# Kernel tuning notes

Measured on AMD Instinct MI355X. Metric: run time of the kernel, lower is better.

## Reference

```python
import jax, jax.numpy as jnp
import numpy as np

B = 4096  # number of graphs (segments)
H = 256   # hidden_aff = hidden_comp = hidden_prot
NEG = -1e30

def leaky(x):
    return jax.nn.leaky_relu(x, 0.1)

def _lin(key, fin, fout):
    k1, k2 = jax.random.split(key)
    lim = 1.0 / np.sqrt(fin)
    W = jax.random.uniform(k1, (fin, fout), jnp.float32, -lim, lim)
    b = jax.random.uniform(k2, (fout,), jnp.float32, -lim, lim)
    return W, b

def setup_inputs() -> dict:
    key = jax.random.key(0)
    ks = jax.random.split(key, 16)
    N = 262144
    comp_feature = jax.random.normal(ks[0], (N, H), jnp.float32)
    prot_feature = jax.random.normal(ks[1], (N, H), jnp.float32)
    batch_comp = jnp.sort(jax.random.randint(ks[2], (N,), 0, B, jnp.int32))
    batch_prot = jnp.sort(jax.random.randint(ks[3], (N,), 0, B, jnp.int32))
    c_aff_W, c_aff_b = _lin(ks[4], H, H)
    c_sup_W, c_sup_b = _lin(ks[5], H, H)
    p_aff_W, p_aff_b = _lin(ks[6], H, H)
    raw_W1, raw_b1 = _lin(ks[7], 3 * H, H)
    raw_W2, raw_b2 = _lin(ks[8], H, H)
    alpha_W1, alpha_b1 = _lin(ks[9], 3 * H, H)
    alpha_W2, alpha_b2 = _lin(ks[10], H, 1)
    out_W1, out_b1 = _lin(ks[11], H, H)
    out_W2, out_b2 = _lin(ks[12], H, 1)
    return dict(comp_feature=comp_feature, prot_feature=prot_feature,
                batch_comp=batch_comp, batch_prot=batch_prot,
                c_aff_W=c_aff_W, c_aff_b=c_aff_b, c_sup_W=c_sup_W, c_sup_b=c_sup_b,
                p_aff_W=p_aff_W, p_aff_b=p_aff_b,
                raw_W1=raw_W1, raw_b1=raw_b1, raw_W2=raw_W2, raw_b2=raw_b2,
                alpha_W1=alpha_W1, alpha_b1=alpha_b1, alpha_W2=alpha_W2, alpha_b2=alpha_b2,
                out_W1=out_W1, out_b1=out_b1, out_W2=out_W2, out_b2=out_b2)

def reference(comp_feature, prot_feature, batch_comp, batch_prot,
              c_aff_W, c_aff_b, c_sup_W, c_sup_b, p_aff_W, p_aff_b,
              raw_W1, raw_b1, raw_W2, raw_b2,
              alpha_W1, alpha_b1, alpha_W2, alpha_b2,
              out_W1, out_b1, out_W2, out_b2):
    comp_emb = leaky(comp_feature @ c_aff_W + c_aff_b)           # [N, H]
    prot_emb = leaky(prot_feature @ p_aff_W + p_aff_b)           # [N, H]
    prot_pool = jax.ops.segment_max(prot_emb, batch_prot, num_segments=B)  # [B, H]
    supe = jax.ops.segment_sum(leaky(comp_feature @ c_sup_W + c_sup_b),
                               batch_comp, num_segments=B)       # [B, H]
    feat = jnp.concatenate([comp_emb, supe[batch_comp], prot_pool[batch_comp]], axis=1)  # [N, 3H]
    raw = leaky(feat @ raw_W1 + raw_b1) @ raw_W2 + raw_b2        # [N, H]
    prealpha = leaky(feat @ alpha_W1 + alpha_b1) @ alpha_W2 + alpha_b2  # [N, 1]
    # scatter softmax over graphs
    seg_max = jax.ops.segment_max(prealpha, batch_comp, num_segments=B)
    a_exp = jnp.exp(prealpha - seg_max[batch_comp])
    a_sum = jax.ops.segment_sum(a_exp, batch_comp, num_segments=B) + 1e-6
    alpha = a_exp / a_sum[batch_comp]                            # [N, 1]
    vector = jax.ops.segment_sum(raw * alpha, batch_comp, num_segments=B)  # [B, H]
    affinity_pred = leaky(vector @ out_W1 + out_b1) @ out_W2 + out_b2      # [B, 1]
    return vector, alpha, affinity_pred
```

## Files before the change

kernel.cpp:

```cpp
#include <hip/hip_runtime.h>
#include <cstddef>
#include <cstdint>

#define HDIM 256
#define BSEG 4096

typedef __bf16 bf16x8 __attribute__((ext_vector_type(8)));
typedef float f32x4 __attribute__((ext_vector_type(4)));

__device__ __forceinline__ float leaky(float x) { return x >= 0.f ? x : 0.1f * x; }
__device__ __forceinline__ float bf2f(ushort u) {
    return __builtin_bit_cast(float, (uint32_t)u << 16);
}
__device__ __forceinline__ ushort f2bf(float f) {
    uint32_t x = __builtin_bit_cast(uint32_t, f);
    return (ushort)((x + 0x7fffu + ((x >> 16) & 1u)) >> 16);
}
__device__ __forceinline__ bf16x8 pack8(float4 a, float4 b) {
    union { ushort s[8]; bf16x8 v; } u;
    u.s[0] = f2bf(a.x); u.s[1] = f2bf(a.y); u.s[2] = f2bf(a.z); u.s[3] = f2bf(a.w);
    u.s[4] = f2bf(b.x); u.s[5] = f2bf(b.y); u.s[6] = f2bf(b.z); u.s[7] = f2bf(b.w);
    return u.v;
}
__device__ __forceinline__ void store_bf4(ushort* p, float v0, float v1, float v2, float v3) {
    ushort4 o; o.x = f2bf(v0); o.y = f2bf(v1); o.z = f2bf(v2); o.w = f2bf(v3);
    *(ushort4*)p = o;
}

__device__ __forceinline__ void gld16(const ushort* g, ushort* lds) {
    __builtin_amdgcn_global_load_lds(
        (const __attribute__((address_space(1))) uint32_t*)g,
        (__attribute__((address_space(3))) uint32_t*)lds, 16, 0, 0);
}
__device__ __forceinline__ void gld16f(const float* g, float* lds) {
    __builtin_amdgcn_global_load_lds(
        (const __attribute__((address_space(1))) uint32_t*)g,
        (__attribute__((address_space(3))) uint32_t*)lds, 16, 0, 0);
}

__global__ void seg_bounds_k(const int* __restrict__ bc, const int* __restrict__ bp,
                             int* __restrict__ sc, int* __restrict__ sp, int n, int nb)
{
    int t = blockIdx.x * blockDim.x + threadIdx.x;
    if (t >= 2 * (nb + 1)) return;
    bool isc = (t <= nb);
    const int* a = isc ? bc : bp;
    int v = isc ? t : t - (nb + 1);
    int lo = 0, hi = n;
    while (lo < hi) { int mid = (lo + hi) >> 1; if (a[mid] < v) lo = mid + 1; else hi = mid; }
    if (isc) sc[t] = lo; else sp[t - (nb + 1)] = lo;
}

__global__ __launch_bounds__(256) void wt_cast_all(
    const float* __restrict__ s0, const float* __restrict__ s1,
    const float* __restrict__ s2, const float* __restrict__ s3,
    const float* __restrict__ s4, const float* __restrict__ s5,
    ushort* __restrict__ d0, ushort* __restrict__ d1, ushort* __restrict__ d2,
    ushort* __restrict__ d3, ushort* __restrict__ d4, ushort* __restrict__ d5)
{
    int m = blockIdx.x >> 4, tile = blockIdx.x & 15;
    const float* s = m == 0 ? s0 : m == 1 ? s1 : m == 2 ? s2 : m == 3 ? s3 : m == 4 ? s4 : s5;
    ushort*      d = m == 0 ? d0 : m == 1 ? d1 : m == 2 ? d2 : m == 3 ? d3 : m == 4 ? d4 : d5;
    int r0 = (tile >> 2) * 64, c0 = (tile & 3) * 64;
    __shared__ ushort t[64][72];
    int cc = threadIdx.x & 63, rr = threadIdx.x >> 6;
    for (int r = rr; r < 64; r += 4) t[cc][r] = f2bf(s[(size_t)(r0 + r) * 256 + c0 + cc]);
    __syncthreads();
    for (int r = rr; r < 64; r += 4) d[(size_t)(c0 + r) * 256 + r0 + cc] = t[r][cc];
}

template<bool LEAKYACT, bool ROWBIAS, bool AFP32, bool ALPHADOT, int YT>
__global__ __launch_bounds__(512) void mg2(
    const void* __restrict__ Av, const ushort* __restrict__ WT,
    const float* __restrict__ bias0, const float* __restrict__ bias1,
    const float* __restrict__ rt0, const float* __restrict__ rt1,
    const int* __restrict__ idx,
    ushort* __restrict__ out0, ushort* __restrict__ out1,
    const float* __restrict__ w2, float* __restrict__ pre)
{
    __shared__ __attribute__((aligned(16))) ushort Bs[2][256 * 32];
    __shared__ __attribute__((aligned(16))) char AsRaw[2][AFP32 ? 128 * 32 * 4 : 128 * 32 * 2];
    __shared__ float pb[128][4];

    const int tid = threadIdx.x;
    const int l = tid & 63, w = tid >> 6;

    const uint nwg = gridDim.x, orig = blockIdx.x;
    const uint swz = (orig & 7) * (nwg >> 3) + (orig >> 3);
    const int bx = (int)(swz / YT), cb = (int)(swz % YT);
    const int row0 = bx * 128, colb = cb * 256;

    const float*  Af = (const float*)Av;
    const ushort* Ah = (const ushort*)Av;

    const int sB0 = w * 128 + l;
    const int rB0 = sB0 >> 2,        rB1 = (sB0 + 64) >> 2;
    const int qB0 = (sB0 & 3) ^ ((rB0 >> 1) & 3), qB1 = ((sB0 + 64) & 3) ^ ((rB1 >> 1) & 3);
    const ushort* srcB0 = WT + (size_t)(colb + rB0) * HDIM + qB0 * 8;
    const ushort* srcB1 = WT + (size_t)(colb + rB1) * HDIM + qB1 * 8;
    const int sA0 = w * 128 + l;
    const int rA0 = sA0 >> 3,        rA1 = (sA0 + 64) >> 3;
    const int qA0 = (sA0 & 7) ^ (rA0 & 7), qA1 = ((sA0 + 64) & 7) ^ (rA1 & 7);
    const float* fsrc0 = Af + (size_t)(row0 + rA0) * HDIM + qA0 * 4;
    const float* fsrc1 = Af + (size_t)(row0 + rA1) * HDIM + qA1 * 4;
    const int rH = tid >> 2, qH = (tid & 3) ^ ((rH >> 1) & 3);
    const ushort* hsrc = Ah + (size_t)(row0 + rH) * HDIM + qH * 8;

    const int wr = (w >> 2) * 64, wc = (w & 3) * 64;
    const int lr = l & 15, lt = l >> 4;

    f32x4 acc[4][4] = {};

#define STAGE(buf, k0) do { \
        gld16(srcB0 + (k0), &Bs[buf][sB0 * 8]); \
        gld16(srcB1 + (k0), &Bs[buf][(sB0 + 64) * 8]); \
        if (AFP32) { \
            gld16f(fsrc0 + (k0), &((float*)AsRaw[buf])[sA0 * 4]); \
            gld16f(fsrc1 + (k0), &((float*)AsRaw[buf])[(sA0 + 64) * 4]); \
        } else { \
            gld16(hsrc + (k0), &((ushort*)AsRaw[buf])[tid * 8]); \
        } \
    } while (0)

#define COMPUTE(buf) do { \
        bf16x8 af[4], bv[4]; \
        _Pragma("unroll") \
        for (int m = 0; m < 4; ++m) { \
            const int row = wr + m * 16 + lr; \
            if (AFP32) { \
                const float* Ab = (const float*)AsRaw[buf]; \
                const int q0 = (2 * lt) ^ (row & 7), q1 = (2 * lt + 1) ^ (row & 7); \
                float4 x = *(const float4*)&Ab[row * 32 + q0 * 4]; \
                float4 y = *(const float4*)&Ab[row * 32 + q1 * 4]; \
                af[m] = pack8(x, y); \
            } else { \
                const ushort* Ab = (const ushort*)AsRaw[buf]; \
                const int q = lt ^ ((row >> 1) & 3); \
                af[m] = *(const bf16x8*)&Ab[row * 32 + q * 8]; \
            } \
        } \
        _Pragma("unroll") \
        for (int n = 0; n < 4; ++n) { \
            const int brow = wc + n * 16 + lr; \
            const int q = lt ^ ((brow >> 1) & 3); \
            bv[n] = *(const bf16x8*)&Bs[buf][brow * 32 + q * 8]; \
        } \
        _Pragma("unroll") \
        for (int m = 0; m < 4; ++m) \
            _Pragma("unroll") \
            for (int n = 0; n < 4; ++n) \
                acc[m][n] = __builtin_amdgcn_mfma_f32_16x16x32_bf16(bv[n], af[m], acc[m][n], 0, 0, 0); \
    } while (0)

    STAGE(0, 0);
    __syncthreads();
    int cur = 0;
    #pragma unroll
    for (int t = 1; t < 8; ++t) {
        STAGE(cur ^ 1, t * 32);
        COMPUTE(cur);
        __syncthreads();
        cur ^= 1;
    }
    COMPUTE(cur);

#undef STAGE
#undef COMPUTE

    if (ALPHADOT && cb == 1) {
        #pragma unroll
        for (int m = 0; m < 4; ++m) {
            const int row = row0 + wr + m * 16 + lr;
            const float* rrow = rt1 + (size_t)idx[row] * HDIM;
            float p = 0.f;
            #pragma unroll
            for (int n = 0; n < 4; ++n) {
                const int c = wc + n * 16 + (lt << 2);
                float4 r4 = *(const float4*)&rrow[c];
                float4 w4 = *(const float4*)&w2[c];
                float v0 = acc[m][n][0] + r4.x, v1 = acc[m][n][1] + r4.y;
                float v2 = acc[m][n][2] + r4.z, v3 = acc[m][n][3] + r4.w;
                if (LEAKYACT) { v0 = leaky(v0); v1 = leaky(v1); v2 = leaky(v2); v3 = leaky(v3); }
                p += v0 * w4.x + v1 * w4.y + v2 * w4.z + v3 * w4.w;
            }
            p += __shfl_xor(p, 16);
            p += __shfl_xor(p, 32);
            if (lt == 0) pb[wr + m * 16 + lr][w & 3] = p;
        }
        __syncthreads();
        if (tid < 128) pre[row0 + tid] = pb[tid][0] + pb[tid][1] + pb[tid][2] + pb[tid][3];
    } else {
        const float* bias = (YT == 2 && cb == 1) ? bias1 : bias0;
        const float* rtab = (YT == 2 && cb == 1) ? rt1 : rt0;
        ushort* outp = (YT == 2 && cb == 1) ? out1 : out0;
        #pragma unroll
        for (int m = 0; m < 4; ++m) {
            const int row = row0 + wr + m * 16 + lr;
            const float* rrow = nullptr;
            if (ROWBIAS) rrow = rtab + (size_t)idx[row] * HDIM;
            #pragma unroll
            for (int n = 0; n < 4; ++n) {
                const int c = wc + n * 16 + (lt << 2);
                float v0 = acc[m][n][0], v1 = acc[m][n][1], v2 = acc[m][n][2], v3 = acc[m][n][3];
                if (bias) {
                    float4 b4 = *(const float4*)&bias[c];
                    v0 += b4.x; v1 += b4.y; v2 += b4.z; v3 += b4.w;
                }
                if (ROWBIAS) {
                    float4 r4 = *(const float4*)&rrow[c];
                    v0 += r4.x; v1 += r4.y; v2 += r4.z; v3 += r4.w;
                }
                if (LEAKYACT) { v0 = leaky(v0); v1 = leaky(v1); v2 = leaky(v2); v3 = leaky(v3); }
                store_bf4(&outp[(size_t)row * HDIM + c], v0, v1, v2, v3);
            }
        }
    }
}

__global__ __launch_bounds__(256) void gemm64_2(
    const float* __restrict__ A, const float* __restrict__ A2,
    const float* __restrict__ Wb_r, const float* __restrict__ Wc_r, const float* __restrict__ bias_r,
    const float* __restrict__ Wb_a, const float* __restrict__ Wc_a, const float* __restrict__ bias_a,
    float* __restrict__ Cr, float* __restrict__ Ca)
{
    const int K = HDIM, NO = HDIM;
    const float* W  = blockIdx.z ? Wb_a : Wb_r;
    const float* W2 = blockIdx.z ? Wc_a : Wc_r;
    const float* bias = blockIdx.z ? bias_a : bias_r;
    float* C = blockIdx.z ? Ca : Cr;

    __shared__ float As [16][68];
    __shared__ float Bs [16][68];
    __shared__ float As2[16][68];
    __shared__ float Bs2[16][68];

    const int tid = threadIdx.x;
    const int tx = tid & 15, ty = tid >> 4;
    const int row0 = blockIdx.x * 64, col0 = blockIdx.y * 64;

    const int lr = tid >> 2;
    const int lk = (tid & 3) << 2;
    const int bk = tid >> 4;
    const int bj = (tid & 15) << 2;

    float acc[4][4] = {};

    for (int k0 = 0; k0 < K; k0 += 16) {
        float4 a4 = *(const float4*)&A[(size_t)(row0 + lr) * K + k0 + lk];
        As[lk + 0][lr] = a4.x; As[lk + 1][lr] = a4.y;
        As[lk + 2][lr] = a4.z; As[lk + 3][lr] = a4.w;
        *(float4*)&Bs[bk][bj] = *(const float4*)&W[(size_t)(k0 + bk) * NO + col0 + bj];
        float4 c4 = *(const float4*)&A2[(size_t)(row0 + lr) * K + k0 + lk];
        As2[lk + 0][lr] = c4.x; As2[lk + 1][lr] = c4.y;
        As2[lk + 2][lr] = c4.z; As2[lk + 3][lr] = c4.w;
        *(float4*)&Bs2[bk][bj] = *(const float4*)&W2[(size_t)(k0 + bk) * NO + col0 + bj];
        __syncthreads();
        #pragma unroll
        for (int kk = 0; kk < 16; ++kk) {
            float4 av = *(const float4*)&As[kk][ty << 2];
            float4 bv = *(const float4*)&Bs[kk][tx << 2];
            float a_[4] = {av.x, av.y, av.z, av.w};
            float b_[4] = {bv.x, bv.y, bv.z, bv.w};
            #pragma unroll
            for (int i = 0; i < 4; ++i)
                #pragma unroll
                for (int j = 0; j < 4; ++j)
                    acc[i][j] += a_[i] * b_[j];
            float4 av2 = *(const float4*)&As2[kk][ty << 2];
            float4 bv2 = *(const float4*)&Bs2[kk][tx << 2];
            float c_[4] = {av2.x, av2.y, av2.z, av2.w};
            float d_[4] = {bv2.x, bv2.y, bv2.z, bv2.w};
            #pragma unroll
            for (int i = 0; i < 4; ++i)
                #pragma unroll
                for (int j = 0; j < 4; ++j)
                    acc[i][j] += c_[i] * d_[j];
        }
        __syncthreads();
    }

    #pragma unroll
    for (int i = 0; i < 4; ++i) {
        int row = row0 + (ty << 2) + i;
        float vv[4];
        #pragma unroll
        for (int j = 0; j < 4; ++j) {
            int col = col0 + (tx << 2) + j;
            vv[j] = acc[i][j] + bias[col];
        }
        float4 o; o.x = vv[0]; o.y = vv[1]; o.z = vv[2]; o.w = vv[3];
        *(float4*)&C[(size_t)row * NO + col0 + (tx << 2)] = o;
    }
}

template<bool ISMAX>
__global__ __launch_bounds__(256) void seg_reduce8(const ushort* __restrict__ in,
        const int* __restrict__ starts, float* __restrict__ out)
{
    __shared__ float part[8][HDIM];
    const int b = blockIdx.x, tid = threadIdx.x;
    const int sub = tid & 31, r = tid >> 5;
    const int s = starts[b], e = starts[b + 1];
    float a[8];
    #pragma unroll
    for (int j = 0; j < 8; ++j) a[j] = ISMAX ? -INFINITY : 0.f;
    for (int i = s + r; i < e; i += 8) {
        uint4 v = *(const uint4*)&in[(size_t)i * HDIM + sub * 8];
        float f[8] = { bf2f((ushort)v.x), bf2f((ushort)(v.x >> 16)),
                       bf2f((ushort)v.y), bf2f((ushort)(v.y >> 16)),
                       bf2f((ushort)v.z), bf2f((ushort)(v.z >> 16)),
                       bf2f((ushort)v.w), bf2f((ushort)(v.w >> 16)) };
        #pragma unroll
        for (int j = 0; j < 8; ++j) a[j] = ISMAX ? fmaxf(a[j], f[j]) : (a[j] + f[j]);
    }
    #pragma unroll
    for (int j = 0; j < 8; ++j) part[r][sub * 8 + j] = a[j];
    __syncthreads();
    float res = part[0][tid];
    #pragma unroll
    for (int j = 1; j < 8; ++j) res = ISMAX ? fmaxf(res, part[j][tid]) : (res + part[j][tid]);
    out[(size_t)b * HDIM + tid] = res;
}

__global__ __launch_bounds__(64) void seg_softmax_k(const float* __restrict__ pre,
        const int* __restrict__ starts, float* __restrict__ alpha)
{
    int b = blockIdx.x, lane = threadIdx.x;
    int s = starts[b], e = starts[b + 1];
    float m = -INFINITY;
    for (int i = s + lane; i < e; i += 64) m = fmaxf(m, pre[i]);
    #pragma unroll
    for (int off = 32; off; off >>= 1) m = fmaxf(m, __shfl_xor(m, off));
    float sum = 0.f;
    for (int i = s + lane; i < e; i += 64) sum += expf(pre[i] - m);
    #pragma unroll
    for (int off = 32; off; off >>= 1) sum += __shfl_xor(sum, off);
    sum += 1e-6f;
    for (int i = s + lane; i < e; i += 64) alpha[i] = expf(pre[i] - m) / sum;
}

__global__ __launch_bounds__(256) void seg_wsum8(const ushort* __restrict__ raw,
        const float* __restrict__ alpha, const int* __restrict__ starts,
        float* __restrict__ vec)
{
    __shared__ float part[8][HDIM];
    const int b = blockIdx.x, tid = threadIdx.x;
    const int sub = tid & 31, r = tid >> 5;
    const int s = starts[b], e = starts[b + 1];
    float a[8] = {};
    for (int i = s + r; i < e; i += 8) {
        float al = alpha[i];
        uint4 v = *(const uint4*)&raw[(size_t)i * HDIM + sub * 8];
        a[0] += bf2f((ushort)v.x) * al;        a[1] += bf2f((ushort)(v.x >> 16)) * al;
        a[2] += bf2f((ushort)v.y) * al;        a[3] += bf2f((ushort)(v.y >> 16)) * al;
        a[4] += bf2f((ushort)v.z) * al;        a[5] += bf2f((ushort)(v.z >> 16)) * al;
        a[6] += bf2f((ushort)v.w) * al;        a[7] += bf2f((ushort)(v.w >> 16)) * al;
    }
    #pragma unroll
    for (int j = 0; j < 8; ++j) part[r][sub * 8 + j] = a[j];
    __syncthreads();
    float res = 0.f;
    #pragma unroll
    for (int j = 0; j < 8; ++j) res += part[j][tid];
    vec[(size_t)b * HDIM + tid] = res;
}

__global__ __launch_bounds__(256) void affinity_k(const float* __restrict__ vec,
        const float* __restrict__ W1, const float* __restrict__ b1,
        const float* __restrict__ W2, const float* __restrict__ b2,
        float* __restrict__ out)
{
    __shared__ float v[HDIM];
    __shared__ float red[4];
    int b = blockIdx.x, t = threadIdx.x;
    v[t] = vec[(size_t)b * HDIM + t];
    __syncthreads();
    float h = 0.f;
    #pragma unroll 8
    for (int k = 0; k < HDIM; ++k) h += v[k] * W1[(size_t)k * HDIM + t];
    h += b1[t];
    h = leaky(h);
    float p = h * W2[t];
    #pragma unroll
    for (int off = 32; off; off >>= 1) p += __shfl_down(p, off);
    int lane = t & 63, wid = t >> 6;
    if (lane == 0) red[wid] = p;
    __syncthreads();
    if (t == 0) out[b] = red[0] + red[1] + red[2] + red[3] + b2[0];
}

extern "C" void kernel_launch(void* const* d_in, const int* in_sizes, int n_in,
                              void* d_out, int out_size, void* d_ws, size_t ws_size,
                              hipStream_t stream)
{
    const int N = in_sizes[2];
    const int H = HDIM;
    const int B = BSEG;

    const float* comp   = (const float*)d_in[0];
    const float* prot   = (const float*)d_in[1];
    const int*   bc     = (const int*)d_in[2];
    const int*   bp     = (const int*)d_in[3];
    const float* c_aff_W = (const float*)d_in[4];
    const float* c_aff_b = (const float*)d_in[5];
    const float* c_sup_W = (const float*)d_in[6];
    const float* c_sup_b = (const float*)d_in[7];
    const float* p_aff_W = (const float*)d_in[8];
    const float* p_aff_b = (const float*)d_in[9];
    const float* raw_W1  = (const float*)d_in[10];
    const float* raw_b1  = (const float*)d_in[11];
    const float* raw_W2  = (const float*)d_in[12];
    const float* raw_b2  = (const float*)d_in[13];
    const float* alpha_W1 = (const float*)d_in[14];
    const float* alpha_b1 = (const float*)d_in[15];
    const float* alpha_W2 = (const float*)d_in[16];
    const float* out_W1  = (const float*)d_in[18];
    const float* out_b1  = (const float*)d_in[19];
    const float* out_W2  = (const float*)d_in[20];
    const float* out_b2  = (const float*)d_in[21];

    const size_t NBIG = (size_t)N * H;
    const size_t SSEG = (size_t)B * H;

    char* p = (char*)d_ws;
    ushort* e1 = (ushort*)p; p += NBIG * 2;
    ushort* e2 = (ushort*)p; p += NBIG * 2;
    ushort* e3 = (ushort*)p; p += NBIG * 2;
    float* supe = (float*)p;  p += SSEG * 4;
    float* pool = (float*)p;  p += SSEG * 4;
    float* gr   = (float*)p;  p += SSEG * 4;
    float* ga   = (float*)p;  p += SSEG * 4;
    float* pre  = (float*)p;  p += (size_t)N * 4;
    ushort* WT1 = (ushort*)p; p += (size_t)512 * 256 * 2;
    ushort* WTp = (ushort*)p; p += (size_t)256 * 256 * 2;
    ushort* WT2 = (ushort*)p; p += (size_t)512 * 256 * 2;
    ushort* WTr = (ushort*)p; p += (size_t)256 * 256 * 2;
    int* sc = (int*)p; p += (size_t)(B + 1) * 4;
    int* sp = (int*)p; p += (size_t)(B + 1) * 4;
    if ((size_t)(p - (char*)d_ws) > ws_size) return;

    ushort* h1   = e3;
    ushort* rawb = e2;

    float* out_vec   = (float*)d_out;
    float* out_alpha = out_vec + SSEG;
    float* out_aff   = out_alpha + N;

    dim3 blk(256), blk5(512);

    seg_bounds_k<<<(2 * (B + 1) + 255) / 256, blk, 0, stream>>>(bc, bp, sc, sp, N, B);
    wt_cast_all<<<6 * 16, blk, 0, stream>>>(
        c_aff_W, c_sup_W, p_aff_W, raw_W1, alpha_W1, raw_W2,
        WT1, WT1 + 65536, WTp, WT2, WT2 + 65536, WTr);

    mg2<true, false, true, false, 2><<<dim3(N / 128 * 2), blk5, 0, stream>>>(
        comp, WT1, c_aff_b, c_sup_b, nullptr, nullptr, nullptr, e1, e2, nullptr, nullptr);
    mg2<true, false, true, false, 1><<<dim3(N / 128), blk5, 0, stream>>>(
        prot, WTp, p_aff_b, nullptr, nullptr, nullptr, nullptr, e3, nullptr, nullptr, nullptr);
    seg_reduce8<false><<<B, blk, 0, stream>>>(e2, sc, supe);
    seg_reduce8<true ><<<B, blk, 0, stream>>>(e3, sp, pool);
    gemm64_2<<<dim3(B / 64, 4, 2), blk, 0, stream>>>(supe, pool,
        raw_W1 + H * H, raw_W1 + 2 * H * H, raw_b1,
        alpha_W1 + H * H, alpha_W1 + 2 * H * H, alpha_b1, gr, ga);
    mg2<true, true, false, true, 2><<<dim3(N / 128 * 2), blk5, 0, stream>>>(
        e1, WT2, nullptr, nullptr, gr, ga, bc, h1, nullptr, alpha_W2, pre);
    seg_softmax_k<<<B, dim3(64), 0, stream>>>(pre, sc, out_alpha);
    mg2<false, false, false, false, 1><<<dim3(N / 128), blk5, 0, stream>>>(
        h1, WTr, raw_b2, nullptr, nullptr, nullptr, nullptr, rawb, nullptr, nullptr, nullptr);
    seg_wsum8<<<B, blk, 0, stream>>>(rawb, out_alpha, sc, out_vec);
    affinity_k<<<B, blk, 0, stream>>>(out_vec, out_W1, out_b1, out_W2, out_b2, out_aff);
}
```

Baseline: 755.1 us.

## Reorder raw_W2 after segment weighted sum and convert fp32 A tiles to bf16

The raw_W2 projection is linear, so the alpha-weighted segment sum is now taken over the hidden activations h1 first. The W2 matmul then runs per graph on B rows instead of N rows, with raw_b2 scaled by the alpha mass per segment, which the softmax kernel now writes out. This removes one full N×256×256 GEMM and its intermediate buffer. Separately, fp32 A operands are now read into registers, converted to bf16 and written to LDS once per tile, halving LDS footprint and removing per-MFMA repacking, at the cost of losing async global-to-LDS loads for A.

```diff
diff --git a/kernel.cpp b/kernel.cpp
--- a/kernel.cpp
+++ b/kernel.cpp
@@ -28,11 +28,6 @@
 }
 
 __device__ __forceinline__ void gld16(const ushort* g, ushort* lds) {
-    __builtin_amdgcn_global_load_lds(
-        (const __attribute__((address_space(1))) uint32_t*)g,
-        (__attribute__((address_space(3))) uint32_t*)lds, 16, 0, 0);
-}
-__device__ __forceinline__ void gld16f(const float* g, float* lds) {
     __builtin_amdgcn_global_load_lds(
         (const __attribute__((address_space(1))) uint32_t*)g,
         (__attribute__((address_space(3))) uint32_t*)lds, 16, 0, 0);
@@ -54,13 +49,13 @@
 __global__ __launch_bounds__(256) void wt_cast_all(
     const float* __restrict__ s0, const float* __restrict__ s1,
     const float* __restrict__ s2, const float* __restrict__ s3,
-    const float* __restrict__ s4, const float* __restrict__ s5,
+    const float* __restrict__ s4,
     ushort* __restrict__ d0, ushort* __restrict__ d1, ushort* __restrict__ d2,
-    ushort* __restrict__ d3, ushort* __restrict__ d4, ushort* __restrict__ d5)
+    ushort* __restrict__ d3, ushort* __restrict__ d4)
 {
     int m = blockIdx.x >> 4, tile = blockIdx.x & 15;
-    const float* s = m == 0 ? s0 : m == 1 ? s1 : m == 2 ? s2 : m == 3 ? s3 : m == 4 ? s4 : s5;
-    ushort*      d = m == 0 ? d0 : m == 1 ? d1 : m == 2 ? d2 : m == 3 ? d3 : m == 4 ? d4 : d5;
+    const float* s = m == 0 ? s0 : m == 1 ? s1 : m == 2 ? s2 : m == 3 ? s3 : s4;
+    ushort*      d = m == 0 ? d0 : m == 1 ? d1 : m == 2 ? d2 : m == 3 ? d3 : d4;
     int r0 = (tile >> 2) * 64, c0 = (tile & 3) * 64;
     __shared__ ushort t[64][72];
     int cc = threadIdx.x & 63, rr = threadIdx.x >> 6;
@@ -70,7 +65,7 @@
 }
 
 template<bool LEAKYACT, bool ROWBIAS, bool AFP32, bool ALPHADOT, int YT>
-__global__ __launch_bounds__(512) void mg2(
+__global__ __launch_bounds__(512) void mg3(
     const void* __restrict__ Av, const ushort* __restrict__ WT,
     const float* __restrict__ bias0, const float* __restrict__ bias1,
     const float* __restrict__ rt0, const float* __restrict__ rt1,
@@ -79,7 +74,7 @@
     const float* __restrict__ w2, float* __restrict__ pre)
 {
     __shared__ __attribute__((aligned(16))) ushort Bs[2][256 * 32];
-    __shared__ __attribute__((aligned(16))) char AsRaw[2][AFP32 ? 128 * 32 * 4 : 128 * 32 * 2];
+    __shared__ __attribute__((aligned(16))) ushort As[2][128 * 32];
     __shared__ float pb[128][4];
 
     const int tid = threadIdx.x;
@@ -98,28 +93,19 @@
     const int qB0 = (sB0 & 3) ^ ((rB0 >> 1) & 3), qB1 = ((sB0 + 64) & 3) ^ ((rB1 >> 1) & 3);
     const ushort* srcB0 = WT + (size_t)(colb + rB0) * HDIM + qB0 * 8;
     const ushort* srcB1 = WT + (size_t)(colb + rB1) * HDIM + qB1 * 8;
-    const int sA0 = w * 128 + l;
-    const int rA0 = sA0 >> 3,        rA1 = (sA0 + 64) >> 3;
-    const int qA0 = (sA0 & 7) ^ (rA0 & 7), qA1 = ((sA0 + 64) & 7) ^ (rA1 & 7);
-    const float* fsrc0 = Af + (size_t)(row0 + rA0) * HDIM + qA0 * 4;
-    const float* fsrc1 = Af + (size_t)(row0 + rA1) * HDIM + qA1 * 4;
-    const int rH = tid >> 2, qH = (tid & 3) ^ ((rH >> 1) & 3);
-    const ushort* hsrc = Ah + (size_t)(row0 + rH) * HDIM + qH * 8;
+    const int srow = tid >> 2, sj = tid & 3;
+    const int lj = sj ^ ((srow >> 1) & 3);
+    const float*  fsrcA = Af + (size_t)(row0 + srow) * HDIM + lj * 8;
+    const ushort* hsrcA = Ah + (size_t)(row0 + srow) * HDIM + lj * 8;
 
     const int wr = (w >> 2) * 64, wc = (w & 3) * 64;
     const int lr = l & 15, lt = l >> 4;
 
     f32x4 acc[4][4] = {};
 
-#define STAGE(buf, k0) do { \
+#define STAGE_B(buf, k0) do { \
         gld16(srcB0 + (k0), &Bs[buf][sB0 * 8]); \
         gld16(srcB1 + (k0), &Bs[buf][(sB0 + 64) * 8]); \
-        if (AFP32) { \
-            gld16f(fsrc0 + (k0), &((float*)AsRaw[buf])[sA0 * 4]); \
-            gld16f(fsrc1 + (k0), &((float*)AsRaw[buf])[(sA0 + 64) * 4]); \
-        } else { \
-            gld16(hsrc + (k0), &((ushort*)AsRaw[buf])[tid * 8]); \
-        } \
     } while (0)
 
 #define COMPUTE(buf) do { \
@@ -127,17 +113,8 @@
         _Pragma("unroll") \
         for (int m = 0; m < 4; ++m) { \
             const int row = wr + m * 16 + lr; \
-            if (AFP32) { \
-                const float* Ab = (const float*)AsRaw[buf]; \
-                const int q0 = (2 * lt) ^ (row & 7), q1 = (2 * lt + 1) ^ (row & 7); \
-                float4 x = *(const float4*)&Ab[row * 32 + q0 * 4]; \
-                float4 y = *(const float4*)&Ab[row * 32 + q1 * 4]; \
-                af[m] = pack8(x, y); \
-            } else { \
-                const ushort* Ab = (const ushort*)AsRaw[buf]; \
-                const int q = lt ^ ((row >> 1) & 3); \
-                af[m] = *(const bf16x8*)&Ab[row * 32 + q * 8]; \
-            } \
+            const int q = lt ^ ((row >> 1) & 3); \
+            af[m] = *(const bf16x8*)&As[buf][row * 32 + q * 8]; \
         } \
         _Pragma("unroll") \
         for (int n = 0; n < 4; ++n) { \
@@ -152,19 +129,41 @@
                 acc[m][n] = __builtin_amdgcn_mfma_f32_16x16x32_bf16(bv[n], af[m], acc[m][n], 0, 0, 0); \
     } while (0)
 
-    STAGE(0, 0);
-    __syncthreads();
     int cur = 0;
-    #pragma unroll
-    for (int t = 1; t < 8; ++t) {
-        STAGE(cur ^ 1, t * 32);
+    if (AFP32) {
+        float4 av0, av1;
+        av0 = *(const float4*)(fsrcA + 0);
+        av1 = *(const float4*)(fsrcA + 4);
+        STAGE_B(0, 0);
+        *(bf16x8*)&As[0][tid * 8] = pack8(av0, av1);
+        __syncthreads();
+        #pragma unroll
+        for (int t = 1; t < 8; ++t) {
+            av0 = *(const float4*)(fsrcA + t * 32);
+            av1 = *(const float4*)(fsrcA + t * 32 + 4);
+            STAGE_B(cur ^ 1, t * 32);
+            COMPUTE(cur);
+            *(bf16x8*)&As[cur ^ 1][tid * 8] = pack8(av0, av1);
+            __syncthreads();
+            cur ^= 1;
+        }
         COMPUTE(cur);
+    } else {
+        STAGE_B(0, 0);
+        gld16(hsrcA, &As[0][tid * 8]);
         __syncthreads();
-        cur ^= 1;
-    }
-    COMPUTE(cur);
-
-#undef STAGE
+        #pragma unroll
+        for (int t = 1; t < 8; ++t) {
+            STAGE_B(cur ^ 1, t * 32);
+            gld16(hsrcA + t * 32, &As[cur ^ 1][tid * 8]);
+            COMPUTE(cur);
+            __syncthreads();
+            cur ^= 1;
+        }
+        COMPUTE(cur);
+    }
+
+#undef STAGE_B
 #undef COMPUTE
 
     if (ALPHADOT && cb == 1) {
@@ -323,7 +322,7 @@
 }
 
 __global__ __launch_bounds__(64) void seg_softmax_k(const float* __restrict__ pre,
-        const int* __restrict__ starts, float* __restrict__ alpha)
+        const int* __restrict__ starts, float* __restrict__ alpha, float* __restrict__ sa)
 {
     int b = blockIdx.x, lane = threadIdx.x;
     int s = starts[b], e = starts[b + 1];
@@ -331,12 +330,13 @@
     for (int i = s + lane; i < e; i += 64) m = fmaxf(m, pre[i]);
     #pragma unroll
     for (int off = 32; off; off >>= 1) m = fmaxf(m, __shfl_xor(m, off));
-    float sum = 0.f;
-    for (int i = s + lane; i < e; i += 64) sum += expf(pre[i] - m);
-    #pragma unroll
-    for (int off = 32; off; off >>= 1) sum += __shfl_xor(sum, off);
-    sum += 1e-6f;
-    for (int i = s + lane; i < e; i += 64) alpha[i] = expf(pre[i] - m) / sum;
+    float S = 0.f;
+    for (int i = s + lane; i < e; i += 64) S += expf(pre[i] - m);
+    #pragma unroll
+    for (int off = 32; off; off >>= 1) S += __shfl_xor(S, off);
+    float denom = S + 1e-6f;
+    if (lane == 0) sa[b] = S / denom;
+    for (int i = s + lane; i < e; i += 64) alpha[i] = expf(pre[i] - m) / denom;
 }
 
 __global__ __launch_bounds__(256) void seg_wsum8(const ushort* __restrict__ raw,
@@ -365,28 +365,36 @@
     vec[(size_t)b * HDIM + tid] = res;
 }
 
-__global__ __launch_bounds__(256) void affinity_k(const float* __restrict__ vec,
-        const float* __restrict__ W1, const float* __restrict__ b1,
-        const float* __restrict__ W2, const float* __restrict__ b2,
-        float* __restrict__ out)
+__global__ __launch_bounds__(256) void final_k(
+    const float* __restrict__ hw, const float* __restrict__ sa,
+    const float* __restrict__ W2r, const float* __restrict__ rb2,
+    const float* __restrict__ oW1, const float* __restrict__ ob1,
+    const float* __restrict__ oW2, const float* __restrict__ ob2,
+    float* __restrict__ out_vec, float* __restrict__ out_aff)
 {
     __shared__ float v[HDIM];
+    __shared__ float vecs[HDIM];
     __shared__ float red[4];
     int b = blockIdx.x, t = threadIdx.x;
-    v[t] = vec[(size_t)b * HDIM + t];
-    __syncthreads();
-    float h = 0.f;
+    v[t] = hw[(size_t)b * HDIM + t];
+    __syncthreads();
+    float a = rb2[t] * sa[b];
     #pragma unroll 8
-    for (int k = 0; k < HDIM; ++k) h += v[k] * W1[(size_t)k * HDIM + t];
-    h += b1[t];
+    for (int k = 0; k < HDIM; ++k) a += v[k] * W2r[(size_t)k * HDIM + t];
+    out_vec[(size_t)b * HDIM + t] = a;
+    vecs[t] = a;
+    __syncthreads();
+    float h = ob1[t];
+    #pragma unroll 8
+    for (int k = 0; k < HDIM; ++k) h += vecs[k] * oW1[(size_t)k * HDIM + t];
     h = leaky(h);
-    float p = h * W2[t];
+    float p = h * oW2[t];
     #pragma unroll
     for (int off = 32; off; off >>= 1) p += __shfl_down(p, off);
     int lane = t & 63, wid = t >> 6;
     if (lane == 0) red[wid] = p;
     __syncthreads();
-    if (t == 0) out[b] = red[0] + red[1] + red[2] + red[3] + b2[0];
+    if (t == 0) out_aff[b] = red[0] + red[1] + red[2] + red[3] + ob2[0];
 }
 
 extern "C" void kernel_launch(void* const* d_in, const int* in_sizes, int n_in,
@@ -430,17 +438,17 @@
     float* pool = (float*)p;  p += SSEG * 4;
     float* gr   = (float*)p;  p += SSEG * 4;
     float* ga   = (float*)p;  p += SSEG * 4;
+    float* hw   = (float*)p;  p += SSEG * 4;
+    float* sa   = (float*)p;  p += (size_t)B * 4;
     float* pre  = (float*)p;  p += (size_t)N * 4;
     ushort* WT1 = (ushort*)p; p += (size_t)512 * 256 * 2;
     ushort* WTp = (ushort*)p; p += (size_t)256 * 256 * 2;
     ushort* WT2 = (ushort*)p; p += (size_t)512 * 256 * 2;
-    ushort* WTr = (ushort*)p; p += (size_t)256 * 256 * 2;
     int* sc = (int*)p; p += (size_t)(B + 1) * 4;
     int* sp = (int*)p; p += (size_t)(B + 1) * 4;
     if ((size_t)(p - (char*)d_ws) > ws_size) return;
 
-    ushort* h1   = e3;
-    ushort* rawb = e2;
+    ushort* h1 = e3;
 
     float* out_vec   = (float*)d_out;
     float* out_alpha = out_vec + SSEG;
@@ -449,24 +457,23 @@
     dim3 blk(256), blk5(512);
 
     seg_bounds_k<<<(2 * (B + 1) + 255) / 256, blk, 0, stream>>>(bc, bp, sc, sp, N, B);
-    wt_cast_all<<<6 * 16, blk, 0, stream>>>(
-        c_aff_W, c_sup_W, p_aff_W, raw_W1, alpha_W1, raw_W2,
-        WT1, WT1 + 65536, WTp, WT2, WT2 + 65536, WTr);
-
-    mg2<true, false, true, false, 2><<<dim3(N / 128 * 2), blk5, 0, stream>>>(
+    wt_cast_all<<<5 * 16, blk, 0, stream>>>(
+        c_aff_W, c_sup_W, p_aff_W, raw_W1, alpha_W1,
+        WT1, WT1 + 65536, WTp, WT2, WT2 + 65536);
+
+    mg3<true, false, true, false, 2><<<dim3(N / 128 * 2), blk5, 0, stream>>>(
         comp, WT1, c_aff_b, c_sup_b, nullptr, nullptr, nullptr, e1, e2, nullptr, nullptr);
-    mg2<true, false, true, false, 1><<<dim3(N / 128), blk5, 0, stream>>>(
+    mg3<true, false, true, false, 1><<<dim3(N / 128), blk5, 0, stream>>>(
         prot, WTp, p_aff_b, nullptr, nullptr, nullptr, nullptr, e3, nullptr, nullptr, nullptr);
     seg_reduce8<false><<<B, blk, 0, stream>>>(e2, sc, supe);
     seg_reduce8<true ><<<B, blk, 0, stream>>>(e3, sp, pool);
     gemm64_2<<<dim3(B / 64, 4, 2), blk, 0, stream>>>(supe, pool,
         raw_W1 + H * H, raw_W1 + 2 * H * H, raw_b1,
         alpha_W1 + H * H, alpha_W1 + 2 * H * H, alpha_b1, gr, ga);
-    mg2<true, true, false, true, 2><<<dim3(N / 128 * 2), blk5, 0, stream>>>(
+    mg3<true, true, false, true, 2><<<dim3(N / 128 * 2), blk5, 0, stream>>>(
         e1, WT2, nullptr, nullptr, gr, ga, bc, h1, nullptr, alpha_W2, pre);
-    seg_softmax_k<<<B, dim3(64), 0, stream>>>(pre, sc, out_alpha);
-    mg2<false, false, false, false, 1><<<dim3(N / 128), blk5, 0, stream>>>(
-        h1, WTr, raw_b2, nullptr, nullptr, nullptr, nullptr, rawb, nullptr, nullptr, nullptr);
-    seg_wsum8<<<B, blk, 0, stream>>>(rawb, out_alpha, sc, out_vec);
-    affinity_k<<<B, blk, 0, stream>>>(out_vec, out_W1, out_b1, out_W2, out_b2, out_aff);
-}
+    seg_softmax_k<<<B, dim3(64), 0, stream>>>(pre, sc, out_alpha, sa);
+    seg_wsum8<<<B, blk, 0, stream>>>(h1, out_alpha, sc, hw);
+    final_k<<<B, blk, 0, stream>>>(hw, sa, raw_W2, raw_b2,
+        out_W1, out_b1, out_W2, out_b2, out_vec, out_aff);
+}
```

Result: faster. 686.3 us (-9.1%).
